# Kernel tuning notes

Measured on AMD Instinct MI355X. Metric: run time of the kernel, lower is better.

The kernel has to match this reference:

```python
import jax, jax.numpy as jnp
import numpy as np

D, H, L, FF, EPS = 3, 3, 12, 2048, 1e-5
B, C, T = 32, 2, 64


def _ln(x, g, b):
    m = jnp.mean(x, -1, keepdims=True)
    v = jnp.mean((x - m) ** 2, -1, keepdims=True)
    return (x - m) / jnp.sqrt(v + EPS) * g + b


def _mha(xq, xkv, w, b, ow, ob):
    # xq: [Tq,B,D], xkv: [S,B,D]; w: [3D,D] packed q/k/v like torch in_proj_weight
    Tq, Bb, _ = xq.shape
    S = xkv.shape[0]
    q = xq @ w[:D].T + b[:D]
    k = xkv @ w[D:2 * D].T + b[D:2 * D]
    v = xkv @ w[2 * D:].T + b[2 * D:]
    dh = D // H  # = 1
    q = q.reshape(Tq, Bb, H, dh)
    k = k.reshape(S, Bb, H, dh)
    v = v.reshape(S, Bb, H, dh)
    scores = jnp.einsum('qbhd,kbhd->bhqk', q, k) * (1.0 / np.sqrt(dh))
    att = jax.nn.softmax(scores, axis=-1)
    o = jnp.einsum('bhqk,kbhd->qbhd', att, v).reshape(Tq, Bb, D)
    return o @ ow.T + ob


def _ffn(x, w1, b1, w2, b2):
    return jax.nn.relu(x @ w1.T + b1) @ w2.T + b2


def _encode(x, p):
    def layer(h, pl):
        aw, ab, aow, aob, g1, b1, g2, b2, f1w, f1b, f2w, f2b = pl
        h = _ln(h + _mha(h, h, aw, ab, aow, aob), g1, b1)
        h = _ln(h + _ffn(h, f1w, f1b, f2w, f2b), g2, b2)
        return h, None
    h, _ = jax.lax.scan(layer, x, p)
    return h


def _decode(tgt, mem, p):
    def layer(h, pl):
        (sw, sb, sow, sob, cw, cb, cow, cob,
         g1, b1, g2, b2, g3, b3, f1w, f1b, f2w, f2b) = pl
        h = _ln(h + _mha(h, h, sw, sb, sow, sob), g1, b1)      # self-attn (no mask, as in source)
        h = _ln(h + _mha(h, mem, cw, cb, cow, cob), g2, b2)    # cross-attn
        h = _ln(h + _ffn(h, f1w, f1b, f2w, f2b), g3, b3)
        return h, None
    h, _ = jax.lax.scan(layer, tgt, p)
    return h


def _forward(src, angle, enc_p, enc_ng, enc_nb, dec_p, dec_ng, dec_nb):
    Bb, _, Tt = src.shape
    a = jnp.broadcast_to(angle.reshape(Bb, 1, 1), (Bb, 1, Tt))
    x = jnp.transpose(jnp.concatenate([src, a], axis=1), (2, 0, 1))  # [T,B,3]
    mem = _ln(_encode(x, enc_p), enc_ng, enc_nb)  # encoder memory is loop-invariant

    def dec(o):
        return _ln(_decode(o, mem, dec_p), dec_ng, dec_nb)

    out = jnp.zeros_like(x).at[0].set(x[0])

    def step(o, t):
        pred = dec(o)
        return o.at[t].set(pred[t]), None

    out, _ = jax.lax.scan(step, out, jnp.arange(1, Tt))
    return jnp.transpose(out, (1, 2, 0))  # [B,3,T]


def setup_inputs() -> dict:
    key = jax.random.key(0)
    it = iter(jax.random.split(key, 40))
    def n(shape, s=0.05):
        return jax.random.normal(next(it), shape, dtype=jnp.float32) * s
    inp = {
        'src': jax.random.normal(next(it), (B, C, T), dtype=jnp.float32),
        'angle': jax.random.normal(next(it), (B,), dtype=jnp.float32),
        'enc_attn_w': n((L, 3 * D, D)), 'enc_attn_b': n((L, 3 * D)),
        'enc_attn_ow': n((L, D, D)), 'enc_attn_ob': n((L, D)),
        'enc_ln1_g': jnp.ones((L, D)), 'enc_ln1_b': jnp.zeros((L, D)),
        'enc_ln2_g': jnp.ones((L, D)), 'enc_ln2_b': jnp.zeros((L, D)),
        'enc_ff1_w': n((L, FF, D)), 'enc_ff1_b': n((L, FF)),
        'enc_ff2_w': n((L, D, FF)), 'enc_ff2_b': n((L, D)),
        'enc_norm_g': jnp.ones((D,)), 'enc_norm_b': jnp.zeros((D,)),
        'dec_sa_w': n((L, 3 * D, D)), 'dec_sa_b': n((L, 3 * D)),
        'dec_sa_ow': n((L, D, D)), 'dec_sa_ob': n((L, D)),
        'dec_ca_w': n((L, 3 * D, D)), 'dec_ca_b': n((L, 3 * D)),
        'dec_ca_ow': n((L, D, D)), 'dec_ca_ob': n((L, D)),
        'dec_ln1_g': jnp.ones((L, D)), 'dec_ln1_b': jnp.zeros((L, D)),
        'dec_ln2_g': jnp.ones((L, D)), 'dec_ln2_b': jnp.zeros((L, D)),
        'dec_ln3_g': jnp.ones((L, D)), 'dec_ln3_b': jnp.zeros((L, D)),
        'dec_ff1_w': n((L, FF, D)), 'dec_ff1_b': n((L, FF)),
        'dec_ff2_w': n((L, D, FF)), 'dec_ff2_b': n((L, D)),
        'dec_norm_g': jnp.ones((D,)), 'dec_norm_b': jnp.zeros((D,)),
    }
    return inp


def reference(src, angle,
              enc_attn_w, enc_attn_b, enc_attn_ow, enc_attn_ob,
              enc_ln1_g, enc_ln1_b, enc_ln2_g, enc_ln2_b,
              enc_ff1_w, enc_ff1_b, enc_ff2_w, enc_ff2_b,
              enc_norm_g, enc_norm_b,
              dec_sa_w, dec_sa_b, dec_sa_ow, dec_sa_ob,
              dec_ca_w, dec_ca_b, dec_ca_ow, dec_ca_ob,
              dec_ln1_g, dec_ln1_b, dec_ln2_g, dec_ln2_b, dec_ln3_g, dec_ln3_b,
              dec_ff1_w, dec_ff1_b, dec_ff2_w, dec_ff2_b,
              dec_norm_g, dec_norm_b):
    enc_p = (enc_attn_w, enc_attn_b, enc_attn_ow, enc_attn_ob,
             enc_ln1_g, enc_ln1_b, enc_ln2_g, enc_ln2_b,
             enc_ff1_w, enc_ff1_b, enc_ff2_w, enc_ff2_b)
    dec_p = (dec_sa_w, dec_sa_b, dec_sa_ow, dec_sa_ob,
             dec_ca_w, dec_ca_b, dec_ca_ow, dec_ca_ob,
             dec_ln1_g, dec_ln1_b, dec_ln2_g, dec_ln2_b, dec_ln3_g, dec_ln3_b,
             dec_ff1_w, dec_ff1_b, dec_ff2_w, dec_ff2_b)
    return _forward(src, angle, enc_p, enc_norm_g, enc_norm_b, dec_p, dec_norm_g, dec_norm_b)
```

## Files before the change

kernel.cpp:

```cpp
#include <hip/hip_runtime.h>

#define DEV static __device__ __forceinline__

typedef _Float16 h2 __attribute__((ext_vector_type(2)));

DEV float fdot2f(h2 a, h2 b, float c) {
#if __has_builtin(__builtin_amdgcn_fdot2)
  return __builtin_amdgcn_fdot2(a, b, c, false);
#else
  return c + (float)a.x * (float)b.x + (float)a.y * (float)b.y;
#endif
}

DEV void ln3(float& a, float& b, float& c, const float* g, const float* bt) {
  float m = (a + b + c) * (1.0f / 3.0f);
  float d0 = a - m, d1 = b - m, d2 = c - m;
  float v = (d0 * d0 + d1 * d1 + d2 * d2) * (1.0f / 3.0f);
  float rs = rsqrtf(v + 1e-5f);
  a = fmaf(d0 * rs, g[0], bt[0]);
  b = fmaf(d1 * rs, g[1], bt[1]);
  c = fmaf(d2 * rs, g[2], bt[2]);
}

DEV unsigned pkh2(float a, float b) {
  h2 v = {(_Float16)a, (_Float16)b};
  return __builtin_bit_cast(unsigned, v);
}

__global__ void __launch_bounds__(256) prepack_kernel(
    const float* ea_w, const float* ea_b, const float* ea_ow, const float* ea_ob,
    const float* el1g, const float* el1b, const float* el2g, const float* el2b,
    const float* ef1w, const float* ef1b, const float* ef2w, const float* ef2b,
    const float* eng, const float* enb,
    const float* dsw, const float* dsb, const float* dsow, const float* dsob,
    const float* dcw, const float* dcb, const float* dcow, const float* dcob,
    const float* dl1g, const float* dl1b, const float* dl2g, const float* dl2b,
    const float* dl3g, const float* dl3b,
    const float* df1w, const float* df1b, const float* df2w, const float* df2b,
    const float* dng, const float* dnb,
    float* ws) {
  const int l = blockIdx.x, tid = threadIdx.x;
  const bool enc = l < 12;
  const int li = enc ? l : l - 12;
  const float* f1w = (enc ? ef1w : df1w) + li * 2048 * 3;
  const float* f1b = (enc ? ef1b : df1b) + li * 2048;
  const float* f2w = (enc ? ef2w : df2w) + li * 3 * 2048;
  uint4* FA4 = (uint4*)ws + (size_t)l * 1024;
  uint4* FB4 = (uint4*)ws + 24 * 1024 + (size_t)l * 1024;
  for (int jp = tid; jp < 1024; jp += 256) {
    const int j0 = jp * 2, j1 = j0 + 1;
    uint4 A;
    A.x = pkh2(f1w[j0 * 3 + 0], f1w[j1 * 3 + 0]);
    A.y = pkh2(f1w[j0 * 3 + 1], f1w[j1 * 3 + 1]);
    A.z = pkh2(f1w[j0 * 3 + 2], f1w[j1 * 3 + 2]);
    A.w = pkh2(f1b[j0], f1b[j1]);
    FA4[jp] = A;
    uint4 Bv;
    Bv.x = pkh2(f2w[j0], f2w[j1]);
    Bv.y = pkh2(f2w[2048 + j0], f2w[2048 + j1]);
    Bv.z = pkh2(f2w[4096 + j0], f2w[4096 + j1]);
    Bv.w = 0u;
    FB4[jp] = Bv;
  }
  float* S = ws + 196608 + l * 128;
  if (tid == 0) {
    const float* aw = (enc ? ea_w : dsw) + li * 27;
    const float* ab = (enc ? ea_b : dsb) + li * 9;
    const float* aow = (enc ? ea_ow : dsow) + li * 9;
    const float* aob = (enc ? ea_ob : dsob) + li * 3;
    for (int i = 0; i < 27; ++i) S[i] = aw[i];
    for (int i = 0; i < 9; ++i) S[27 + i] = ab[i];
    for (int i = 0; i < 9; ++i) S[36 + i] = aow[i];
    for (int i = 0; i < 3; ++i) S[45 + i] = aob[i];
    const float* p;
    p = (enc ? el1g : dl1g) + li * 3; for (int i = 0; i < 3; ++i) S[48 + i] = p[i];
    p = (enc ? el1b : dl1b) + li * 3; for (int i = 0; i < 3; ++i) S[51 + i] = p[i];
    p = (enc ? el2g : dl2g) + li * 3; for (int i = 0; i < 3; ++i) S[54 + i] = p[i];
    p = (enc ? el2b : dl2b) + li * 3; for (int i = 0; i < 3; ++i) S[57 + i] = p[i];
    p = (enc ? ef2b : df2b) + li * 3; for (int i = 0; i < 3; ++i) S[60 + i] = p[i];
    if (!enc) {
      const float* cw = dcw + li * 27;
      for (int i = 0; i < 9; ++i) {
        S[64 + i] = cw[i];
        S[94 + i] = cw[9 + i];
        S[106 + i] = cw[18 + i];
      }
      const float* cb = dcb + li * 9;
      for (int i = 0; i < 3; ++i) {
        S[73 + i] = cb[i];
        S[103 + i] = cb[3 + i];
        S[115 + i] = cb[6 + i];
      }
      for (int i = 0; i < 9; ++i) S[76 + i] = dcow[li * 9 + i];
      for (int i = 0; i < 3; ++i) S[85 + i] = dcob[li * 3 + i];
      p = dl3g + li * 3; for (int i = 0; i < 3; ++i) S[88 + i] = p[i];
      p = dl3b + li * 3; for (int i = 0; i < 3; ++i) S[91 + i] = p[i];
    }
  }
  if (l == 0 && tid == 1) {
    float* G = ws + 196608 + 24 * 128;
    for (int i = 0; i < 3; ++i) {
      G[i] = eng[i]; G[3 + i] = enb[i];
      G[6 + i] = dng[i]; G[9 + i] = dnb[i];
    }
  }
}

template <int NR>
DEV void ffn_core(const uint4* FA, const uint4* FB,
                  const float (&X0)[4], const float (&X1)[4], const float (&X2)[4],
                  float (&acc)[4][3], int lane) {
  h2 xd0[NR], xd1[NR], xd2[NR];
#pragma unroll
  for (int i = 0; i < NR; ++i) {
    xd0[i] = h2{(_Float16)X0[i], (_Float16)X0[i]};
    xd1[i] = h2{(_Float16)X1[i], (_Float16)X1[i]};
    xd2[i] = h2{(_Float16)X2[i], (_Float16)X2[i]};
  }
#pragma unroll
  for (int i = 0; i < NR; ++i) { acc[i][0] = 0.f; acc[i][1] = 0.f; acc[i][2] = 0.f; }
  const h2 z = {(_Float16)0, (_Float16)0};
#pragma unroll 4
  for (int kk = 0; kk < 16; ++kk) {
    const int jp = lane + (kk << 6);
    uint4 a = FA[jp];
    uint4 c = FB[jp];
    h2 wa0 = __builtin_bit_cast(h2, a.x), wa1 = __builtin_bit_cast(h2, a.y);
    h2 wa2 = __builtin_bit_cast(h2, a.z), bb = __builtin_bit_cast(h2, a.w);
    h2 wc0 = __builtin_bit_cast(h2, c.x), wc1 = __builtin_bit_cast(h2, c.y);
    h2 wc2 = __builtin_bit_cast(h2, c.z);
#pragma unroll
    for (int i = 0; i < NR; ++i) {
      h2 t = wa0 * xd0[i] + wa1 * xd1[i] + wa2 * xd2[i] + bb;
      t = __builtin_elementwise_max(t, z);
      acc[i][0] = fdot2f(wc0, t, acc[i][0]);
      acc[i][1] = fdot2f(wc1, t, acc[i][1]);
      acc[i][2] = fdot2f(wc2, t, acc[i][2]);
    }
  }
#pragma unroll
  for (int m = 1; m < 64; m <<= 1) {
#pragma unroll
    for (int i = 0; i < NR; ++i) {
      acc[i][0] += __shfl_xor(acc[i][0], m, 64);
      acc[i][1] += __shfl_xor(acc[i][1], m, 64);
      acc[i][2] += __shfl_xor(acc[i][2], m, 64);
    }
  }
}

template <bool DEC>
DEV void run_layer(const float* sm, const uint4* FA, const uint4* FB,
                   const float (*ckv)[8],
                   float (*h)[5], float (*hln)[5], float* kvq,
                   float (*p1)[25], float (*p2)[25],
                   float (*o_s)[5], const float* glob,
                   int R, int t, bool from_os, bool wpred,
                   int wave, int lane, int tid) {
  {
    const int r = tid >> 4, o = tid & 15;
    if (r < R && o <= 9) {
      float x0, x1, x2;
      if (DEC && from_os) {
        const bool real = r < t;
        x0 = real ? o_s[r][0] : 0.f;
        x1 = real ? o_s[r][1] : 0.f;
        x2 = real ? o_s[r][2] : 0.f;
      } else {
        x0 = h[r][0]; x1 = h[r][1]; x2 = h[r][2];
      }
      if (o < 9) {
        float v = fmaf(sm[o * 3], x0,
                  fmaf(sm[o * 3 + 1], x1, fmaf(sm[o * 3 + 2], x2, sm[27 + o])));
        kvq[r * 13 + o + o / 3] = v;
      } else {
        kvq[r * 13 + 7] = (DEC && r == R - 1 && t > 0) ? (float)(64 - t) : 1.0f;
        if (DEC && from_os) { h[r][0] = x0; h[r][1] = x1; h[r][2] = x2; }
      }
    }
    if (DEC && o == 9 && r >= R) kvq[r * 13 + 7] = 0.f;
  }
  __syncthreads();
  if (wave < 12) {
    const int hd = wave % 3, c = wave / 3;
    const int p0 = c * 16;
    float den = 0.f, num = 0.f;
    if (p0 < R) {
      const float q = kvq[lane * 13 + hd] * 1.44269504f;
#pragma unroll
      for (int pp = 0; pp < 16; ++pp) {
        const int p = p0 + pp;
        float e = exp2f(q * kvq[p * 13 + 4 + hd]);
        if (DEC) e *= kvq[p * 13 + 7];
        den += e;
        num = fmaf(e, kvq[p * 13 + 8 + hd], num);
      }
    }
    p1[lane][2 * wave] = den;
    p1[lane][2 * wave + 1] = num;
  }
  __syncthreads();
  if (DEC) {
    if (wave < 12) {
      const int r = lane, hd = wave % 3, c = wave / 3;
      float d0 = p1[r][0] + p1[r][6] + p1[r][12] + p1[r][18];
      float n0 = p1[r][1] + p1[r][7] + p1[r][13] + p1[r][19];
      float d1 = p1[r][2] + p1[r][8] + p1[r][14] + p1[r][20];
      float n1 = p1[r][3] + p1[r][9] + p1[r][15] + p1[r][21];
      float d2 = p1[r][4] + p1[r][10] + p1[r][16] + p1[r][22];
      float n2 = p1[r][5] + p1[r][11] + p1[r][17] + p1[r][23];
      float oh0 = __fdividef(n0, d0), oh1 = __fdividef(n1, d1), oh2 = __fdividef(n2, d2);
      float a0 = fmaf(sm[36], oh0, fmaf(sm[37], oh1, fmaf(sm[38], oh2, sm[45]))) + h[r][0];
      float a1 = fmaf(sm[39], oh0, fmaf(sm[40], oh1, fmaf(sm[41], oh2, sm[46]))) + h[r][1];
      float a2 = fmaf(sm[42], oh0, fmaf(sm[43], oh1, fmaf(sm[44], oh2, sm[47]))) + h[r][2];
      ln3(a0, a1, a2, sm + 48, sm + 51);
      if (wave == 0 && r < R) { hln[r][0] = a0; hln[r][1] = a1; hln[r][2] = a2; }
      float q = fmaf(sm[64 + hd * 3], a0,
                fmaf(sm[64 + hd * 3 + 1], a1,
                fmaf(sm[64 + hd * 3 + 2], a2, sm[73 + hd]))) * 1.44269504f;
      const int p0 = c * 16;
      float den = 0.f, num = 0.f;
#pragma unroll
      for (int pp = 0; pp < 16; ++pp) {
        const int p = p0 + pp;
        float e = exp2f(q * ckv[p][hd]);
        den += e;
        num = fmaf(e, ckv[p][3 + hd], num);
      }
      p2[r][2 * wave] = den;
      p2[r][2 * wave + 1] = num;
    }
    __syncthreads();
  }
  {
    const int nr = (wave < R) ? (1 + (R - 1 - wave) / 16) : 0;
    if (nr > 0) {
      const float(*pp)[25] = DEC ? p2 : p1;
      const float* ow = DEC ? sm + 76 : sm + 36;
      const float* ob = DEC ? sm + 85 : sm + 45;
      const float* lg = DEC ? sm + 54 : sm + 48;
      const float* lb = DEC ? sm + 57 : sm + 51;
      float X0[4], X1[4], X2[4];
#pragma unroll
      for (int i = 0; i < 4; ++i) {
        X0[i] = 0.f; X1[i] = 0.f; X2[i] = 0.f;
        if (i < nr) {
          const int rc = wave + 16 * i;
          float d0 = pp[rc][0] + pp[rc][6] + pp[rc][12] + pp[rc][18];
          float n0 = pp[rc][1] + pp[rc][7] + pp[rc][13] + pp[rc][19];
          float d1 = pp[rc][2] + pp[rc][8] + pp[rc][14] + pp[rc][20];
          float n1 = pp[rc][3] + pp[rc][9] + pp[rc][15] + pp[rc][21];
          float d2 = pp[rc][4] + pp[rc][10] + pp[rc][16] + pp[rc][22];
          float n2 = pp[rc][5] + pp[rc][11] + pp[rc][17] + pp[rc][23];
          float oh0 = __fdividef(n0, d0), oh1 = __fdividef(n1, d1), oh2 = __fdividef(n2, d2);
          float hr0, hr1, hr2;
          if (DEC) { hr0 = hln[rc][0]; hr1 = hln[rc][1]; hr2 = hln[rc][2]; }
          else     { hr0 = h[rc][0];   hr1 = h[rc][1];   hr2 = h[rc][2]; }
          float a0 = fmaf(ow[0], oh0, fmaf(ow[1], oh1, fmaf(ow[2], oh2, ob[0]))) + hr0;
          float a1 = fmaf(ow[3], oh0, fmaf(ow[4], oh1, fmaf(ow[5], oh2, ob[1]))) + hr1;
          float a2 = fmaf(ow[6], oh0, fmaf(ow[7], oh1, fmaf(ow[8], oh2, ob[2]))) + hr2;
          ln3(a0, a1, a2, lg, lb);
          X0[i] = a0; X1[i] = a1; X2[i] = a2;
        }
      }
      float acc[4][3];
      switch (nr) {
        case 1: ffn_core<1>(FA, FB, X0, X1, X2, acc, lane); break;
        case 2: ffn_core<2>(FA, FB, X0, X1, X2, acc, lane); break;
        case 3: ffn_core<3>(FA, FB, X0, X1, X2, acc, lane); break;
        default: ffn_core<4>(FA, FB, X0, X1, X2, acc, lane); break;
      }
      if (lane == 0) {
        const float* fg = DEC ? sm + 88 : sm + 54;
        const float* fb = DEC ? sm + 91 : sm + 57;
#pragma unroll
        for (int i = 0; i < 4; ++i) {
          if (i < nr) {
            const int r = wave + 16 * i;
            float y0 = acc[i][0] + sm[60] + X0[i];
            float y1 = acc[i][1] + sm[61] + X1[i];
            float y2 = acc[i][2] + sm[62] + X2[i];
            ln3(y0, y1, y2, fg, fb);
            h[r][0] = y0; h[r][1] = y1; h[r][2] = y2;
            if (DEC && wpred && r == R - 1) {
              ln3(y0, y1, y2, glob + 6, glob + 9);
              o_s[t][0] = y0; o_s[t][1] = y1; o_s[t][2] = y2;
            }
          }
        }
      }
    }
    __syncthreads();
  }
}

__global__ void __launch_bounds__(1024) tf_kernel(const float* src, const float* angle,
                                                  const float* ws, float* out) {
  __shared__ float small_s[24][128];
  __shared__ float glob[16];
  __shared__ float h[64][5];
  __shared__ float hln[64][5];
  __shared__ float kvq[64 * 13];
  __shared__ float part1[64][25];
  __shared__ float part2[64][25];
  __shared__ float o_s[64][5];
  __shared__ float ckcv[12][64][8];
  const int b = blockIdx.x;
  const int tid = threadIdx.x, wave = tid >> 6, lane = tid & 63;
  const uint4* FA = (const uint4*)ws;
  const uint4* FB = (const uint4*)ws + 24 * 1024;
  const float* SM = ws + 196608;
  const float* GB = SM + 24 * 128;
  for (int i = tid; i < 24 * 128; i += 1024) ((float*)small_s)[i] = SM[i];
  if (tid < 16) glob[tid] = GB[tid];
  if (tid < 64) {
    float x0 = src[b * 128 + tid];
    float x1 = src[b * 128 + 64 + tid];
    float x2 = angle[b];
    h[tid][0] = x0; h[tid][1] = x1; h[tid][2] = x2;
    o_s[tid][0] = (tid == 0) ? x0 : 0.f;
    o_s[tid][1] = (tid == 0) ? x1 : 0.f;
    o_s[tid][2] = (tid == 0) ? x2 : 0.f;
  }
  __syncthreads();
  for (int l = 0; l < 12; ++l)
    run_layer<false>(small_s[l], FA + (size_t)l * 1024, FB + (size_t)l * 1024,
                     nullptr, h, hln, kvq, part1, part2, o_s, glob,
                     64, 0, false, false, wave, lane, tid);
  if (tid < 64) {
    float a = h[tid][0], bb = h[tid][1], c = h[tid][2];
    ln3(a, bb, c, glob + 0, glob + 3);
    h[tid][0] = a; h[tid][1] = bb; h[tid][2] = c;
  }
  __syncthreads();
  if (wave < 12) {
    const float* sm = small_s[12 + wave];
    float m0 = h[lane][0], m1 = h[lane][1], m2 = h[lane][2];
    float k0 = fmaf(sm[94], m0, fmaf(sm[95], m1, fmaf(sm[96], m2, sm[103])));
    float k1 = fmaf(sm[97], m0, fmaf(sm[98], m1, fmaf(sm[99], m2, sm[104])));
    float k2 = fmaf(sm[100], m0, fmaf(sm[101], m1, fmaf(sm[102], m2, sm[105])));
    float v0 = fmaf(sm[106], m0, fmaf(sm[107], m1, fmaf(sm[108], m2, sm[115])));
    float v1 = fmaf(sm[109], m0, fmaf(sm[110], m1, fmaf(sm[111], m2, sm[116])));
    float v2 = fmaf(sm[112], m0, fmaf(sm[113], m1, fmaf(sm[114], m2, sm[117])));
    ckcv[wave][lane][0] = k0; ckcv[wave][lane][1] = k1; ckcv[wave][lane][2] = k2;
    ckcv[wave][lane][3] = v0; ckcv[wave][lane][4] = v1; ckcv[wave][lane][5] = v2;
  }
  __syncthreads();
  for (int t = 1; t < 64; ++t) {
    const int R = t + 1;
    for (int l = 0; l < 12; ++l)
      run_layer<true>(small_s[12 + l], FA + (size_t)(12 + l) * 1024,
                      FB + (size_t)(12 + l) * 1024, ckcv[l],
                      h, hln, kvq, part1, part2, o_s, glob, R, t,
                      l == 0, l == 11, wave, lane, tid);
  }
  if (tid < 192) {
    int d = tid / 64, tt = tid % 64;
    out[b * 192 + tid] = o_s[tt][d];
  }
}

extern "C" void kernel_launch(void* const* d_in, const int* in_sizes, int n_in,
                              void* d_out, int out_size, void* d_ws, size_t ws_size,
                              hipStream_t stream) {
  (void)in_sizes; (void)n_in; (void)out_size; (void)ws_size;
  float* ws = (float*)d_ws;
  prepack_kernel<<<24, 256, 0, stream>>>(
      (const float*)d_in[2], (const float*)d_in[3], (const float*)d_in[4], (const float*)d_in[5],
      (const float*)d_in[6], (const float*)d_in[7], (const float*)d_in[8], (const float*)d_in[9],
      (const float*)d_in[10], (const float*)d_in[11], (const float*)d_in[12], (const float*)d_in[13],
      (const float*)d_in[14], (const float*)d_in[15],
      (const float*)d_in[16], (const float*)d_in[17], (const float*)d_in[18], (const float*)d_in[19],
      (const float*)d_in[20], (const float*)d_in[21], (const float*)d_in[22], (const float*)d_in[23],
      (const float*)d_in[24], (const float*)d_in[25], (const float*)d_in[26], (const float*)d_in[27],
      (const float*)d_in[28], (const float*)d_in[29],
      (const float*)d_in[30], (const float*)d_in[31], (const float*)d_in[32], (const float*)d_in[33],
      (const float*)d_in[34], (const float*)d_in[35],
      ws);
  tf_kernel<<<32, 1024, 0, stream>>>((const float*)d_in[0], (const float*)d_in[1], ws,
                                     (float*)d_out);
}
```

Baseline: 6.353 ms.

## Double-buffer FFN weights in LDS with async global-to-LDS prefetch of next layer

Interleaves each layer's packed FFN weight arrays (FA/FB) into one contiguous 2048-entry block in the workspace. Each layer now starts an asynchronous global_load_lds copy of the next layer's block into the other half of a two-slot shared-memory buffer. The FFN core then reads weights from LDS instead of global/L2. This hides weight fetch latency behind the attention and FFN work of the current layer. In exchange it adds 64KB of LDS per block, and correctness depends on the existing barriers waiting for the async LDS writes to finish.

```diff
diff --git a/kernel.cpp b/kernel.cpp
--- a/kernel.cpp
+++ b/kernel.cpp
@@ -45,8 +45,8 @@
   const float* f1w = (enc ? ef1w : df1w) + li * 2048 * 3;
   const float* f1b = (enc ? ef1b : df1b) + li * 2048;
   const float* f2w = (enc ? ef2w : df2w) + li * 3 * 2048;
-  uint4* FA4 = (uint4*)ws + (size_t)l * 1024;
-  uint4* FB4 = (uint4*)ws + 24 * 1024 + (size_t)l * 1024;
+  uint4* FA4 = (uint4*)ws + (size_t)l * 2048;
+  uint4* FB4 = FA4 + 1024;
   for (int jp = tid; jp < 1024; jp += 256) {
     const int j0 = jp * 2, j1 = j0 + 1;
     uint4 A;
@@ -106,8 +106,24 @@
   }
 }
 
+DEV void stage_fab(const uint4* g, uint4* l, int wave, int lane) {
+#if __has_builtin(__builtin_amdgcn_global_load_lds)
+  const int e0 = wave * 64;
+  __builtin_amdgcn_global_load_lds(
+      (const __attribute__((address_space(1))) void*)(g + e0 + lane),
+      (__attribute__((address_space(3))) void*)(l + e0), 16, 0, 0);
+  const int e1 = 1024 + wave * 64;
+  __builtin_amdgcn_global_load_lds(
+      (const __attribute__((address_space(1))) void*)(g + e1 + lane),
+      (__attribute__((address_space(3))) void*)(l + e1), 16, 0, 0);
+#else
+  l[wave * 64 + lane] = g[wave * 64 + lane];
+  l[1024 + wave * 64 + lane] = g[1024 + wave * 64 + lane];
+#endif
+}
+
 template <int NR>
-DEV void ffn_core(const uint4* FA, const uint4* FB,
+DEV void ffn_core(const uint4* FAB,
                   const float (&X0)[4], const float (&X1)[4], const float (&X2)[4],
                   float (&acc)[4][3], int lane) {
   h2 xd0[NR], xd1[NR], xd2[NR];
@@ -123,8 +139,8 @@
 #pragma unroll 4
   for (int kk = 0; kk < 16; ++kk) {
     const int jp = lane + (kk << 6);
-    uint4 a = FA[jp];
-    uint4 c = FB[jp];
+    uint4 a = FAB[jp];
+    uint4 c = FAB[1024 + jp];
     h2 wa0 = __builtin_bit_cast(h2, a.x), wa1 = __builtin_bit_cast(h2, a.y);
     h2 wa2 = __builtin_bit_cast(h2, a.z), bb = __builtin_bit_cast(h2, a.w);
     h2 wc0 = __builtin_bit_cast(h2, c.x), wc1 = __builtin_bit_cast(h2, c.y);
@@ -150,13 +166,15 @@
 }
 
 template <bool DEC>
-DEV void run_layer(const float* sm, const uint4* FA, const uint4* FB,
+DEV void run_layer(const float* sm, const uint4* FAB,
+                   const uint4* stage_src, uint4* stage_dst,
                    const float (*ckv)[8],
                    float (*h)[5], float (*hln)[5], float* kvq,
                    float (*p1)[25], float (*p2)[25],
                    float (*o_s)[5], const float* glob,
                    int R, int t, bool from_os, bool wpred,
                    int wave, int lane, int tid) {
+  stage_fab(stage_src, stage_dst, wave, lane);
   {
     const int r = tid >> 4, o = tid & 15;
     if (r < R && o <= 9) {
@@ -265,10 +283,10 @@
       }
       float acc[4][3];
       switch (nr) {
-        case 1: ffn_core<1>(FA, FB, X0, X1, X2, acc, lane); break;
-        case 2: ffn_core<2>(FA, FB, X0, X1, X2, acc, lane); break;
-        case 3: ffn_core<3>(FA, FB, X0, X1, X2, acc, lane); break;
-        default: ffn_core<4>(FA, FB, X0, X1, X2, acc, lane); break;
+        case 1: ffn_core<1>(FAB, X0, X1, X2, acc, lane); break;
+        case 2: ffn_core<2>(FAB, X0, X1, X2, acc, lane); break;
+        case 3: ffn_core<3>(FAB, X0, X1, X2, acc, lane); break;
+        default: ffn_core<4>(FAB, X0, X1, X2, acc, lane); break;
       }
       if (lane == 0) {
         const float* fg = DEC ? sm + 88 : sm + 54;
@@ -296,6 +314,7 @@
 
 __global__ void __launch_bounds__(1024) tf_kernel(const float* src, const float* angle,
                                                   const float* ws, float* out) {
+  __shared__ uint4 fbuf[2][2048];
   __shared__ float small_s[24][128];
   __shared__ float glob[16];
   __shared__ float h[64][5];
@@ -307,10 +326,10 @@
   __shared__ float ckcv[12][64][8];
   const int b = blockIdx.x;
   const int tid = threadIdx.x, wave = tid >> 6, lane = tid & 63;
-  const uint4* FA = (const uint4*)ws;
-  const uint4* FB = (const uint4*)ws + 24 * 1024;
+  const uint4* FABg = (const uint4*)ws;
   const float* SM = ws + 196608;
   const float* GB = SM + 24 * 128;
+  stage_fab(FABg, fbuf[0], wave, lane);
   for (int i = tid; i < 24 * 128; i += 1024) ((float*)small_s)[i] = SM[i];
   if (tid < 16) glob[tid] = GB[tid];
   if (tid < 64) {
@@ -323,10 +342,15 @@
     o_s[tid][2] = (tid == 0) ? x2 : 0.f;
   }
   __syncthreads();
-  for (int l = 0; l < 12; ++l)
-    run_layer<false>(small_s[l], FA + (size_t)l * 1024, FB + (size_t)l * 1024,
-                     nullptr, h, hln, kvq, part1, part2, o_s, glob,
+  int cc = 0;
+  for (int l = 0; l < 12; ++l) {
+    const int nxt = (l < 11) ? l + 1 : 12;
+    run_layer<false>(small_s[l], fbuf[cc & 1], FABg + (size_t)nxt * 2048,
+                     fbuf[(cc + 1) & 1], nullptr,
+                     h, hln, kvq, part1, part2, o_s, glob,
                      64, 0, false, false, wave, lane, tid);
+    ++cc;
+  }
   if (tid < 64) {
     float a = h[tid][0], bb = h[tid][1], c = h[tid][2];
     ln3(a, bb, c, glob + 0, glob + 3);
@@ -348,11 +372,14 @@
   __syncthreads();
   for (int t = 1; t < 64; ++t) {
     const int R = t + 1;
-    for (int l = 0; l < 12; ++l)
-      run_layer<true>(small_s[12 + l], FA + (size_t)(12 + l) * 1024,
-                      FB + (size_t)(12 + l) * 1024, ckcv[l],
+    for (int li = 0; li < 12; ++li) {
+      const int nxt = (li < 11) ? 12 + li + 1 : 12;
+      run_layer<true>(small_s[12 + li], fbuf[cc & 1], FABg + (size_t)nxt * 2048,
+                      fbuf[(cc + 1) & 1], ckcv[li],
                       h, hln, kvq, part1, part2, o_s, glob, R, t,
-                      l == 0, l == 11, wave, lane, tid);
+                      li == 0, li == 11, wave, lane, tid);
+      ++cc;
+    }
   }
   if (tid < 192) {
     int d = tid / 64, tt = tid % 64;
```

New measurement: 6.463 ms. Within noise of the previous version (+1.7%).

## Restructure attention to 4 waves, batch FFN over 8 waves with more rows

Applied to the files above, without the earlier changes.

Attention now uses 4 waves that each handle all three heads over a 16-key slice, reading keys and values as float4 from transposed shared buffers. The output projection and LayerNorm are computed once by a single wave into a shared buffer, instead of being recomputed per FFN wave. The FFN then runs on 8 waves, each holding up to 8 rows, so every weight load is reused across more rows, and the FA/FB weights are interleaved per layer for locality. The cost is fewer active waves for the FFN weight streaming, plus an extra barrier and serialized single-wave work per layer.

```diff
diff --git a/kernel.cpp b/kernel.cpp
--- a/kernel.cpp
+++ b/kernel.cpp
@@ -45,8 +45,8 @@
   const float* f1w = (enc ? ef1w : df1w) + li * 2048 * 3;
   const float* f1b = (enc ? ef1b : df1b) + li * 2048;
   const float* f2w = (enc ? ef2w : df2w) + li * 3 * 2048;
-  uint4* FA4 = (uint4*)ws + (size_t)l * 1024;
-  uint4* FB4 = (uint4*)ws + 24 * 1024 + (size_t)l * 1024;
+  uint4* FA4 = (uint4*)ws + (size_t)l * 2048;
+  uint4* FB4 = FA4 + 1024;
   for (int jp = tid; jp < 1024; jp += 256) {
     const int j0 = jp * 2, j1 = j0 + 1;
     uint4 A;
@@ -107,9 +107,9 @@
 }
 
 template <int NR>
-DEV void ffn_core(const uint4* FA, const uint4* FB,
-                  const float (&X0)[4], const float (&X1)[4], const float (&X2)[4],
-                  float (&acc)[4][3], int lane) {
+DEV void ffn_core(const uint4* FA,
+                  const float (&X0)[8], const float (&X1)[8], const float (&X2)[8],
+                  float (&acc)[8][3], int lane) {
   h2 xd0[NR], xd1[NR], xd2[NR];
 #pragma unroll
   for (int i = 0; i < NR; ++i) {
@@ -124,7 +124,7 @@
   for (int kk = 0; kk < 16; ++kk) {
     const int jp = lane + (kk << 6);
     uint4 a = FA[jp];
-    uint4 c = FB[jp];
+    uint4 c = FA[1024 + jp];
     h2 wa0 = __builtin_bit_cast(h2, a.x), wa1 = __builtin_bit_cast(h2, a.y);
     h2 wa2 = __builtin_bit_cast(h2, a.z), bb = __builtin_bit_cast(h2, a.w);
     h2 wc0 = __builtin_bit_cast(h2, c.x), wc1 = __builtin_bit_cast(h2, c.y);
@@ -150,133 +150,158 @@
 }
 
 template <bool DEC>
-DEV void run_layer(const float* sm, const uint4* FA, const uint4* FB,
-                   const float (*ckv)[8],
-                   float (*h)[5], float (*hln)[5], float* kvq,
-                   float (*p1)[25], float (*p2)[25],
+DEV void run_layer(const float* sm, const uint4* FA, const float4* ckv4,
+                   float (*h)[5], float (*hln)[5], float (*xs)[5],
+                   float (*kq)[5], float4* kvk, float4* kvv,
+                   float (*p1t)[64], float (*p2t)[64],
                    float (*o_s)[5], const float* glob,
                    int R, int t, bool from_os, bool wpred,
                    int wave, int lane, int tid) {
   {
     const int r = tid >> 4, o = tid & 15;
-    if (r < R && o <= 9) {
-      float x0, x1, x2;
-      if (DEC && from_os) {
-        const bool real = r < t;
-        x0 = real ? o_s[r][0] : 0.f;
-        x1 = real ? o_s[r][1] : 0.f;
-        x2 = real ? o_s[r][2] : 0.f;
-      } else {
-        x0 = h[r][0]; x1 = h[r][1]; x2 = h[r][2];
-      }
-      if (o < 9) {
+    if (o < 9) {
+      if (r < R) {
+        float x0, x1, x2;
+        if (DEC && from_os) {
+          const bool real = r < t;
+          x0 = real ? o_s[r][0] : 0.f;
+          x1 = real ? o_s[r][1] : 0.f;
+          x2 = real ? o_s[r][2] : 0.f;
+        } else {
+          x0 = h[r][0]; x1 = h[r][1]; x2 = h[r][2];
+        }
         float v = fmaf(sm[o * 3], x0,
                   fmaf(sm[o * 3 + 1], x1, fmaf(sm[o * 3 + 2], x2, sm[27 + o])));
-        kvq[r * 13 + o + o / 3] = v;
-      } else {
-        kvq[r * 13 + 7] = (DEC && r == R - 1 && t > 0) ? (float)(64 - t) : 1.0f;
-        if (DEC && from_os) { h[r][0] = x0; h[r][1] = x1; h[r][2] = x2; }
-      }
-    }
-    if (DEC && o == 9 && r >= R) kvq[r * 13 + 7] = 0.f;
-  }
-  __syncthreads();
-  if (wave < 12) {
-    const int hd = wave % 3, c = wave / 3;
-    const int p0 = c * 16;
-    float den = 0.f, num = 0.f;
-    if (p0 < R) {
-      const float q = kvq[lane * 13 + hd] * 1.44269504f;
+        if (o < 3) kq[r][o] = v;
+        else if (o < 6) ((float*)&kvk[r])[o - 3] = v;
+        else ((float*)&kvv[r])[o - 6] = v;
+      } else if (DEC) {
+        if (o < 3) kq[r][o] = 0.f;
+        else if (o < 6) ((float*)&kvk[r])[o - 3] = 0.f;
+        else ((float*)&kvv[r])[o - 6] = 0.f;
+      }
+    } else if (o == 9) {
+      if (DEC)
+        ((float*)&kvk[r])[3] =
+            (r == R - 1 && t > 0) ? (float)(64 - t) : (r < R ? 1.f : 0.f);
+      if (DEC && from_os && r < R) {
+        const bool real = r < t;
+        h[r][0] = real ? o_s[r][0] : 0.f;
+        h[r][1] = real ? o_s[r][1] : 0.f;
+        h[r][2] = real ? o_s[r][2] : 0.f;
+      }
+    }
+  }
+  __syncthreads();
+  if (wave < 4) {
+    const float l2e = 1.44269504f;
+    float q0 = kq[lane][0] * l2e, q1 = kq[lane][1] * l2e, q2 = kq[lane][2] * l2e;
+    float d0 = 0.f, n0 = 0.f, d1 = 0.f, n1 = 0.f, d2 = 0.f, n2 = 0.f;
+    const int p0 = wave * 16;
+#pragma unroll
+    for (int pp = 0; pp < 16; ++pp) {
+      float4 k = kvk[p0 + pp], v = kvv[p0 + pp];
+      float e0 = exp2f(q0 * k.x), e1 = exp2f(q1 * k.y), e2 = exp2f(q2 * k.z);
+      if (DEC) { e0 *= k.w; e1 *= k.w; e2 *= k.w; }
+      d0 += e0; n0 = fmaf(e0, v.x, n0);
+      d1 += e1; n1 = fmaf(e1, v.y, n1);
+      d2 += e2; n2 = fmaf(e2, v.z, n2);
+    }
+    p1t[wave * 6 + 0][lane] = d0; p1t[wave * 6 + 1][lane] = n0;
+    p1t[wave * 6 + 2][lane] = d1; p1t[wave * 6 + 3][lane] = n1;
+    p1t[wave * 6 + 4][lane] = d2; p1t[wave * 6 + 5][lane] = n2;
+  }
+  __syncthreads();
+  if (DEC) {
+    if (wave < 4) {
+      float d0 = p1t[0][lane] + p1t[6][lane] + p1t[12][lane] + p1t[18][lane];
+      float n0 = p1t[1][lane] + p1t[7][lane] + p1t[13][lane] + p1t[19][lane];
+      float d1 = p1t[2][lane] + p1t[8][lane] + p1t[14][lane] + p1t[20][lane];
+      float n1 = p1t[3][lane] + p1t[9][lane] + p1t[15][lane] + p1t[21][lane];
+      float d2 = p1t[4][lane] + p1t[10][lane] + p1t[16][lane] + p1t[22][lane];
+      float n2 = p1t[5][lane] + p1t[11][lane] + p1t[17][lane] + p1t[23][lane];
+      float oh0 = __fdividef(n0, d0), oh1 = __fdividef(n1, d1), oh2 = __fdividef(n2, d2);
+      float a0 = fmaf(sm[36], oh0, fmaf(sm[37], oh1, fmaf(sm[38], oh2, sm[45]))) + h[lane][0];
+      float a1 = fmaf(sm[39], oh0, fmaf(sm[40], oh1, fmaf(sm[41], oh2, sm[46]))) + h[lane][1];
+      float a2 = fmaf(sm[42], oh0, fmaf(sm[43], oh1, fmaf(sm[44], oh2, sm[47]))) + h[lane][2];
+      ln3(a0, a1, a2, sm + 48, sm + 51);
+      if (wave == 0 && lane < R) {
+        hln[lane][0] = a0; hln[lane][1] = a1; hln[lane][2] = a2;
+      }
+      const float l2e = 1.44269504f;
+      float q0 = fmaf(sm[64], a0, fmaf(sm[65], a1, fmaf(sm[66], a2, sm[73]))) * l2e;
+      float q1 = fmaf(sm[67], a0, fmaf(sm[68], a1, fmaf(sm[69], a2, sm[74]))) * l2e;
+      float q2 = fmaf(sm[70], a0, fmaf(sm[71], a1, fmaf(sm[72], a2, sm[75]))) * l2e;
+      float D0 = 0.f, N0 = 0.f, D1 = 0.f, N1 = 0.f, D2 = 0.f, N2 = 0.f;
+      const int p0 = wave * 16;
 #pragma unroll
       for (int pp = 0; pp < 16; ++pp) {
-        const int p = p0 + pp;
-        float e = exp2f(q * kvq[p * 13 + 4 + hd]);
-        if (DEC) e *= kvq[p * 13 + 7];
-        den += e;
-        num = fmaf(e, kvq[p * 13 + 8 + hd], num);
-      }
-    }
-    p1[lane][2 * wave] = den;
-    p1[lane][2 * wave + 1] = num;
-  }
-  __syncthreads();
-  if (DEC) {
-    if (wave < 12) {
-      const int r = lane, hd = wave % 3, c = wave / 3;
-      float d0 = p1[r][0] + p1[r][6] + p1[r][12] + p1[r][18];
-      float n0 = p1[r][1] + p1[r][7] + p1[r][13] + p1[r][19];
-      float d1 = p1[r][2] + p1[r][8] + p1[r][14] + p1[r][20];
-      float n1 = p1[r][3] + p1[r][9] + p1[r][15] + p1[r][21];
-      float d2 = p1[r][4] + p1[r][10] + p1[r][16] + p1[r][22];
-      float n2 = p1[r][5] + p1[r][11] + p1[r][17] + p1[r][23];
-      float oh0 = __fdividef(n0, d0), oh1 = __fdividef(n1, d1), oh2 = __fdividef(n2, d2);
-      float a0 = fmaf(sm[36], oh0, fmaf(sm[37], oh1, fmaf(sm[38], oh2, sm[45]))) + h[r][0];
-      float a1 = fmaf(sm[39], oh0, fmaf(sm[40], oh1, fmaf(sm[41], oh2, sm[46]))) + h[r][1];
-      float a2 = fmaf(sm[42], oh0, fmaf(sm[43], oh1, fmaf(sm[44], oh2, sm[47]))) + h[r][2];
-      ln3(a0, a1, a2, sm + 48, sm + 51);
-      if (wave == 0 && r < R) { hln[r][0] = a0; hln[r][1] = a1; hln[r][2] = a2; }
-      float q = fmaf(sm[64 + hd * 3], a0,
-                fmaf(sm[64 + hd * 3 + 1], a1,
-                fmaf(sm[64 + hd * 3 + 2], a2, sm[73 + hd]))) * 1.44269504f;
-      const int p0 = c * 16;
-      float den = 0.f, num = 0.f;
-#pragma unroll
-      for (int pp = 0; pp < 16; ++pp) {
-        const int p = p0 + pp;
-        float e = exp2f(q * ckv[p][hd]);
-        den += e;
-        num = fmaf(e, ckv[p][3 + hd], num);
-      }
-      p2[r][2 * wave] = den;
-      p2[r][2 * wave + 1] = num;
+        float4 k = ckv4[(p0 + pp) * 2], v = ckv4[(p0 + pp) * 2 + 1];
+        float e0 = exp2f(q0 * k.x), e1 = exp2f(q1 * k.y), e2 = exp2f(q2 * k.z);
+        D0 += e0; N0 = fmaf(e0, v.x, N0);
+        D1 += e1; N1 = fmaf(e1, v.y, N1);
+        D2 += e2; N2 = fmaf(e2, v.z, N2);
+      }
+      p2t[wave * 6 + 0][lane] = D0; p2t[wave * 6 + 1][lane] = N0;
+      p2t[wave * 6 + 2][lane] = D1; p2t[wave * 6 + 3][lane] = N1;
+      p2t[wave * 6 + 4][lane] = D2; p2t[wave * 6 + 5][lane] = N2;
     }
     __syncthreads();
   }
+  if (wave == 0) {
+    const float (*pt)[64] = DEC ? p2t : p1t;
+    float d0 = pt[0][lane] + pt[6][lane] + pt[12][lane] + pt[18][lane];
+    float n0 = pt[1][lane] + pt[7][lane] + pt[13][lane] + pt[19][lane];
+    float d1 = pt[2][lane] + pt[8][lane] + pt[14][lane] + pt[20][lane];
+    float n1 = pt[3][lane] + pt[9][lane] + pt[15][lane] + pt[21][lane];
+    float d2 = pt[4][lane] + pt[10][lane] + pt[16][lane] + pt[22][lane];
+    float n2 = pt[5][lane] + pt[11][lane] + pt[17][lane] + pt[23][lane];
+    float oh0 = __fdividef(n0, d0), oh1 = __fdividef(n1, d1), oh2 = __fdividef(n2, d2);
+    const float* ow = DEC ? sm + 76 : sm + 36;
+    const float* ob = DEC ? sm + 85 : sm + 45;
+    float r0, r1, r2;
+    if (DEC) { r0 = hln[lane][0]; r1 = hln[lane][1]; r2 = hln[lane][2]; }
+    else     { r0 = h[lane][0];   r1 = h[lane][1];   r2 = h[lane][2]; }
+    float a0 = fmaf(ow[0], oh0, fmaf(ow[1], oh1, fmaf(ow[2], oh2, ob[0]))) + r0;
+    float a1 = fmaf(ow[3], oh0, fmaf(ow[4], oh1, fmaf(ow[5], oh2, ob[1]))) + r1;
+    float a2 = fmaf(ow[6], oh0, fmaf(ow[7], oh1, fmaf(ow[8], oh2, ob[2]))) + r2;
+    const float* lg = DEC ? sm + 54 : sm + 48;
+    const float* lb = DEC ? sm + 57 : sm + 51;
+    ln3(a0, a1, a2, lg, lb);
+    if (lane < R) { xs[lane][0] = a0; xs[lane][1] = a1; xs[lane][2] = a2; }
+  }
+  __syncthreads();
   {
-    const int nr = (wave < R) ? (1 + (R - 1 - wave) / 16) : 0;
-    if (nr > 0) {
-      const float(*pp)[25] = DEC ? p2 : p1;
-      const float* ow = DEC ? sm + 76 : sm + 36;
-      const float* ob = DEC ? sm + 85 : sm + 45;
-      const float* lg = DEC ? sm + 54 : sm + 48;
-      const float* lb = DEC ? sm + 57 : sm + 51;
-      float X0[4], X1[4], X2[4];
-#pragma unroll
-      for (int i = 0; i < 4; ++i) {
-        X0[i] = 0.f; X1[i] = 0.f; X2[i] = 0.f;
+    if (wave < 8 && wave < R) {
+      const int nr = (R - wave + 7) >> 3;
+      float X0[8], X1[8], X2[8];
+#pragma unroll
+      for (int i = 0; i < 8; ++i) {
         if (i < nr) {
-          const int rc = wave + 16 * i;
-          float d0 = pp[rc][0] + pp[rc][6] + pp[rc][12] + pp[rc][18];
-          float n0 = pp[rc][1] + pp[rc][7] + pp[rc][13] + pp[rc][19];
-          float d1 = pp[rc][2] + pp[rc][8] + pp[rc][14] + pp[rc][20];
-          float n1 = pp[rc][3] + pp[rc][9] + pp[rc][15] + pp[rc][21];
-          float d2 = pp[rc][4] + pp[rc][10] + pp[rc][16] + pp[rc][22];
-          float n2 = pp[rc][5] + pp[rc][11] + pp[rc][17] + pp[rc][23];
-          float oh0 = __fdividef(n0, d0), oh1 = __fdividef(n1, d1), oh2 = __fdividef(n2, d2);
-          float hr0, hr1, hr2;
-          if (DEC) { hr0 = hln[rc][0]; hr1 = hln[rc][1]; hr2 = hln[rc][2]; }
-          else     { hr0 = h[rc][0];   hr1 = h[rc][1];   hr2 = h[rc][2]; }
-          float a0 = fmaf(ow[0], oh0, fmaf(ow[1], oh1, fmaf(ow[2], oh2, ob[0]))) + hr0;
-          float a1 = fmaf(ow[3], oh0, fmaf(ow[4], oh1, fmaf(ow[5], oh2, ob[1]))) + hr1;
-          float a2 = fmaf(ow[6], oh0, fmaf(ow[7], oh1, fmaf(ow[8], oh2, ob[2]))) + hr2;
-          ln3(a0, a1, a2, lg, lb);
-          X0[i] = a0; X1[i] = a1; X2[i] = a2;
+          const int rc = wave + 8 * i;
+          X0[i] = xs[rc][0]; X1[i] = xs[rc][1]; X2[i] = xs[rc][2];
+        } else {
+          X0[i] = 0.f; X1[i] = 0.f; X2[i] = 0.f;
         }
       }
-      float acc[4][3];
+      float acc[8][3];
       switch (nr) {
-        case 1: ffn_core<1>(FA, FB, X0, X1, X2, acc, lane); break;
-        case 2: ffn_core<2>(FA, FB, X0, X1, X2, acc, lane); break;
-        case 3: ffn_core<3>(FA, FB, X0, X1, X2, acc, lane); break;
-        default: ffn_core<4>(FA, FB, X0, X1, X2, acc, lane); break;
+        case 1: ffn_core<1>(FA, X0, X1, X2, acc, lane); break;
+        case 2: ffn_core<2>(FA, X0, X1, X2, acc, lane); break;
+        case 3: ffn_core<3>(FA, X0, X1, X2, acc, lane); break;
+        case 4: ffn_core<4>(FA, X0, X1, X2, acc, lane); break;
+        case 5: ffn_core<5>(FA, X0, X1, X2, acc, lane); break;
+        case 6: ffn_core<6>(FA, X0, X1, X2, acc, lane); break;
+        case 7: ffn_core<7>(FA, X0, X1, X2, acc, lane); break;
+        default: ffn_core<8>(FA, X0, X1, X2, acc, lane); break;
       }
       if (lane == 0) {
         const float* fg = DEC ? sm + 88 : sm + 54;
         const float* fb = DEC ? sm + 91 : sm + 57;
 #pragma unroll
-        for (int i = 0; i < 4; ++i) {
+        for (int i = 0; i < 8; ++i) {
           if (i < nr) {
-            const int r = wave + 16 * i;
+            const int r = wave + 8 * i;
             float y0 = acc[i][0] + sm[60] + X0[i];
             float y1 = acc[i][1] + sm[61] + X1[i];
             float y2 = acc[i][2] + sm[62] + X2[i];
@@ -300,15 +325,17 @@
   __shared__ float glob[16];
   __shared__ float h[64][5];
   __shared__ float hln[64][5];
-  __shared__ float kvq[64 * 13];
-  __shared__ float part1[64][25];
-  __shared__ float part2[64][25];
+  __shared__ float xs[64][5];
   __shared__ float o_s[64][5];
-  __shared__ float ckcv[12][64][8];
+  __shared__ float kq[64][5];
+  __shared__ __align__(16) float4 kvk[64];
+  __shared__ __align__(16) float4 kvv[64];
+  __shared__ float p1t[24][64];
+  __shared__ float p2t[24][64];
+  __shared__ __align__(16) float ckcv[12][64][8];
   const int b = blockIdx.x;
   const int tid = threadIdx.x, wave = tid >> 6, lane = tid & 63;
-  const uint4* FA = (const uint4*)ws;
-  const uint4* FB = (const uint4*)ws + 24 * 1024;
+  const uint4* FABg = (const uint4*)ws;
   const float* SM = ws + 196608;
   const float* GB = SM + 24 * 128;
   for (int i = tid; i < 24 * 128; i += 1024) ((float*)small_s)[i] = SM[i];
@@ -324,8 +351,8 @@
   }
   __syncthreads();
   for (int l = 0; l < 12; ++l)
-    run_layer<false>(small_s[l], FA + (size_t)l * 1024, FB + (size_t)l * 1024,
-                     nullptr, h, hln, kvq, part1, part2, o_s, glob,
+    run_layer<false>(small_s[l], FABg + (size_t)l * 2048, nullptr,
+                     h, hln, xs, kq, kvk, kvv, p1t, p2t, o_s, glob,
                      64, 0, false, false, wave, lane, tid);
   if (tid < 64) {
     float a = h[tid][0], bb = h[tid][1], c = h[tid][2];
@@ -343,16 +370,18 @@
     float v1 = fmaf(sm[109], m0, fmaf(sm[110], m1, fmaf(sm[111], m2, sm[116])));
     float v2 = fmaf(sm[112], m0, fmaf(sm[113], m1, fmaf(sm[114], m2, sm[117])));
     ckcv[wave][lane][0] = k0; ckcv[wave][lane][1] = k1; ckcv[wave][lane][2] = k2;
-    ckcv[wave][lane][3] = v0; ckcv[wave][lane][4] = v1; ckcv[wave][lane][5] = v2;
+    ckcv[wave][lane][3] = 0.f;
+    ckcv[wave][lane][4] = v0; ckcv[wave][lane][5] = v1; ckcv[wave][lane][6] = v2;
+    ckcv[wave][lane][7] = 0.f;
   }
   __syncthreads();
   for (int t = 1; t < 64; ++t) {
     const int R = t + 1;
-    for (int l = 0; l < 12; ++l)
-      run_layer<true>(small_s[12 + l], FA + (size_t)(12 + l) * 1024,
-                      FB + (size_t)(12 + l) * 1024, ckcv[l],
-                      h, hln, kvq, part1, part2, o_s, glob, R, t,
-                      l == 0, l == 11, wave, lane, tid);
+    for (int li = 0; li < 12; ++li)
+      run_layer<true>(small_s[12 + li], FABg + (size_t)(12 + li) * 2048,
+                      (const float4*)ckcv[li],
+                      h, hln, xs, kq, kvk, kvv, p1t, p2t, o_s, glob, R, t,
+                      li == 0, li == 11, wave, lane, tid);
   }
   if (tid < 192) {
     int d = tid / 64, tt = tid % 64;
```

Measured after the change: 7.575 ms. 19.2% more time.

## Fuse QKV projection into attention waves and drop a barrier per layer

Applied to the files above, without the earlier changes.

Removes the separate QKV projection phase and its __syncthreads by having each attention wave recompute its query, key and value from the hidden state on the fly. Stores the hidden state as float4 for vectorized shared loads. Interleaves the two FFN weight tables per layer into one contiguous region for locality. This trades redundant per-lane projection arithmetic for one fewer barrier per layer across 12×64 layer passes, and the first decoder layer now also has wave 12 write the masked hidden state.

```diff
diff --git a/kernel.cpp b/kernel.cpp
--- a/kernel.cpp
+++ b/kernel.cpp
@@ -45,8 +45,8 @@
   const float* f1w = (enc ? ef1w : df1w) + li * 2048 * 3;
   const float* f1b = (enc ? ef1b : df1b) + li * 2048;
   const float* f2w = (enc ? ef2w : df2w) + li * 3 * 2048;
-  uint4* FA4 = (uint4*)ws + (size_t)l * 1024;
-  uint4* FB4 = (uint4*)ws + 24 * 1024 + (size_t)l * 1024;
+  uint4* FA4 = (uint4*)ws + (size_t)l * 2048;
+  uint4* FB4 = FA4 + 1024;
   for (int jp = tid; jp < 1024; jp += 256) {
     const int j0 = jp * 2, j1 = j0 + 1;
     uint4 A;
@@ -107,7 +107,7 @@
 }
 
 template <int NR>
-DEV void ffn_core(const uint4* FA, const uint4* FB,
+DEV void ffn_core(const uint4* FA,
                   const float (&X0)[4], const float (&X1)[4], const float (&X2)[4],
                   float (&acc)[4][3], int lane) {
   h2 xd0[NR], xd1[NR], xd2[NR];
@@ -124,7 +124,7 @@
   for (int kk = 0; kk < 16; ++kk) {
     const int jp = lane + (kk << 6);
     uint4 a = FA[jp];
-    uint4 c = FB[jp];
+    uint4 c = FA[1024 + jp];
     h2 wa0 = __builtin_bit_cast(h2, a.x), wa1 = __builtin_bit_cast(h2, a.y);
     h2 wa2 = __builtin_bit_cast(h2, a.z), bb = __builtin_bit_cast(h2, a.w);
     h2 wc0 = __builtin_bit_cast(h2, c.x), wc1 = __builtin_bit_cast(h2, c.y);
@@ -150,54 +150,72 @@
 }
 
 template <bool DEC>
-DEV void run_layer(const float* sm, const uint4* FA, const uint4* FB,
-                   const float (*ckv)[8],
-                   float (*h)[5], float (*hln)[5], float* kvq,
+DEV void run_layer(const float* sm, const uint4* FA, const float (*ckv)[8],
+                   float4* hv, float (*hln)[5],
                    float (*p1)[25], float (*p2)[25],
                    float (*o_s)[5], const float* glob,
                    int R, int t, bool from_os, bool wpred,
                    int wave, int lane, int tid) {
-  {
-    const int r = tid >> 4, o = tid & 15;
-    if (r < R && o <= 9) {
-      float x0, x1, x2;
-      if (DEC && from_os) {
-        const bool real = r < t;
-        x0 = real ? o_s[r][0] : 0.f;
-        x1 = real ? o_s[r][1] : 0.f;
-        x2 = real ? o_s[r][2] : 0.f;
-      } else {
-        x0 = h[r][0]; x1 = h[r][1]; x2 = h[r][2];
-      }
-      if (o < 9) {
-        float v = fmaf(sm[o * 3], x0,
-                  fmaf(sm[o * 3 + 1], x1, fmaf(sm[o * 3 + 2], x2, sm[27 + o])));
-        kvq[r * 13 + o + o / 3] = v;
-      } else {
-        kvq[r * 13 + 7] = (DEC && r == R - 1 && t > 0) ? (float)(64 - t) : 1.0f;
-        if (DEC && from_os) { h[r][0] = x0; h[r][1] = x1; h[r][2] = x2; }
-      }
-    }
-    if (DEC && o == 9 && r >= R) kvq[r * 13 + 7] = 0.f;
-  }
-  __syncthreads();
   if (wave < 12) {
     const int hd = wave % 3, c = wave / 3;
     const int p0 = c * 16;
+    const float l2e = 1.44269504f;
+    float xq0, xq1, xq2;
+    if (DEC && from_os) {
+      const bool real = lane < t;
+      xq0 = real ? o_s[lane][0] : 0.f;
+      xq1 = real ? o_s[lane][1] : 0.f;
+      xq2 = real ? o_s[lane][2] : 0.f;
+    } else {
+      float4 hx = hv[lane];
+      xq0 = hx.x; xq1 = hx.y; xq2 = hx.z;
+    }
+    float q = fmaf(sm[hd * 3], xq0,
+              fmaf(sm[hd * 3 + 1], xq1,
+              fmaf(sm[hd * 3 + 2], xq2, sm[27 + hd]))) * l2e;
     float den = 0.f, num = 0.f;
-    if (p0 < R) {
-      const float q = kvq[lane * 13 + hd] * 1.44269504f;
-#pragma unroll
-      for (int pp = 0; pp < 16; ++pp) {
-        const int p = p0 + pp;
-        float e = exp2f(q * kvq[p * 13 + 4 + hd]);
-        if (DEC) e *= kvq[p * 13 + 7];
-        den += e;
-        num = fmaf(e, kvq[p * 13 + 8 + hd], num);
-      }
+#pragma unroll
+    for (int pp = 0; pp < 16; ++pp) {
+      const int p = p0 + pp;
+      float x0, x1, x2, mult;
+      if (DEC && from_os) {
+        const bool real = p < t;
+        x0 = real ? o_s[p][0] : 0.f;
+        x1 = real ? o_s[p][1] : 0.f;
+        x2 = real ? o_s[p][2] : 0.f;
+        mult = (p == R - 1) ? (float)(64 - t) : (p < R ? 1.f : 0.f);
+      } else if (DEC) {
+        const int pc = min(p, R - 1);
+        float4 hx = hv[pc];
+        x0 = hx.x; x1 = hx.y; x2 = hx.z;
+        mult = (p == R - 1) ? (t > 0 ? (float)(64 - t) : 1.f)
+                            : (p < R ? 1.f : 0.f);
+      } else {
+        float4 hx = hv[p];
+        x0 = hx.x; x1 = hx.y; x2 = hx.z;
+        mult = 1.f;
+      }
+      float k = fmaf(sm[9 + hd * 3], x0,
+                fmaf(sm[9 + hd * 3 + 1], x1,
+                fmaf(sm[9 + hd * 3 + 2], x2, sm[30 + hd])));
+      float v = fmaf(sm[18 + hd * 3], x0,
+                fmaf(sm[18 + hd * 3 + 1], x1,
+                fmaf(sm[18 + hd * 3 + 2], x2, sm[33 + hd])));
+      float e = exp2f(q * k);
+      if (DEC) e *= mult;
+      den += e;
+      num = fmaf(e, v, num);
     }
     p1[lane][2 * wave] = den;
     p1[lane][2 * wave + 1] = num;
+  } else if (DEC && from_os && wave == 12) {
+    const bool real = lane < t;
+    float4 hx;
+    hx.x = real ? o_s[lane][0] : 0.f;
+    hx.y = real ? o_s[lane][1] : 0.f;
+    hx.z = real ? o_s[lane][2] : 0.f;
+    hx.w = 0.f;
+    hv[lane] = hx;
   }
   __syncthreads();
   if (DEC) {
@@ -210,9 +228,10 @@
       float d2 = p1[r][4] + p1[r][10] + p1[r][16] + p1[r][22];
       float n2 = p1[r][5] + p1[r][11] + p1[r][17] + p1[r][23];
       float oh0 = __fdividef(n0, d0), oh1 = __fdividef(n1, d1), oh2 = __fdividef(n2, d2);
-      float a0 = fmaf(sm[36], oh0, fmaf(sm[37], oh1, fmaf(sm[38], oh2, sm[45]))) + h[r][0];
-      float a1 = fmaf(sm[39], oh0, fmaf(sm[40], oh1, fmaf(sm[41], oh2, sm[46]))) + h[r][1];
-      float a2 = fmaf(sm[42], oh0, fmaf(sm[43], oh1, fmaf(sm[44], oh2, sm[47]))) + h[r][2];
+      float4 hx = hv[r];
+      float a0 = fmaf(sm[36], oh0, fmaf(sm[37], oh1, fmaf(sm[38], oh2, sm[45]))) + hx.x;
+      float a1 = fmaf(sm[39], oh0, fmaf(sm[40], oh1, fmaf(sm[41], oh2, sm[46]))) + hx.y;
+      float a2 = fmaf(sm[42], oh0, fmaf(sm[43], oh1, fmaf(sm[44], oh2, sm[47]))) + hx.z;
       ln3(a0, a1, a2, sm + 48, sm + 51);
       if (wave == 0 && r < R) { hln[r][0] = a0; hln[r][1] = a1; hln[r][2] = a2; }
       float q = fmaf(sm[64 + hd * 3], a0,
@@ -255,7 +274,7 @@
           float oh0 = __fdividef(n0, d0), oh1 = __fdividef(n1, d1), oh2 = __fdividef(n2, d2);
           float hr0, hr1, hr2;
           if (DEC) { hr0 = hln[rc][0]; hr1 = hln[rc][1]; hr2 = hln[rc][2]; }
-          else     { hr0 = h[rc][0];   hr1 = h[rc][1];   hr2 = h[rc][2]; }
+          else     { float4 hx = hv[rc]; hr0 = hx.x; hr1 = hx.y; hr2 = hx.z; }
           float a0 = fmaf(ow[0], oh0, fmaf(ow[1], oh1, fmaf(ow[2], oh2, ob[0]))) + hr0;
           float a1 = fmaf(ow[3], oh0, fmaf(ow[4], oh1, fmaf(ow[5], oh2, ob[1]))) + hr1;
           float a2 = fmaf(ow[6], oh0, fmaf(ow[7], oh1, fmaf(ow[8], oh2, ob[2]))) + hr2;
@@ -265,10 +284,10 @@
       }
       float acc[4][3];
       switch (nr) {
-        case 1: ffn_core<1>(FA, FB, X0, X1, X2, acc, lane); break;
-        case 2: ffn_core<2>(FA, FB, X0, X1, X2, acc, lane); break;
-        case 3: ffn_core<3>(FA, FB, X0, X1, X2, acc, lane); break;
-        default: ffn_core<4>(FA, FB, X0, X1, X2, acc, lane); break;
+        case 1: ffn_core<1>(FA, X0, X1, X2, acc, lane); break;
+        case 2: ffn_core<2>(FA, X0, X1, X2, acc, lane); break;
+        case 3: ffn_core<3>(FA, X0, X1, X2, acc, lane); break;
+        default: ffn_core<4>(FA, X0, X1, X2, acc, lane); break;
       }
       if (lane == 0) {
         const float* fg = DEC ? sm + 88 : sm + 54;
@@ -281,7 +300,8 @@
             float y1 = acc[i][1] + sm[61] + X1[i];
             float y2 = acc[i][2] + sm[62] + X2[i];
             ln3(y0, y1, y2, fg, fb);
-            h[r][0] = y0; h[r][1] = y1; h[r][2] = y2;
+            float4 hx; hx.x = y0; hx.y = y1; hx.z = y2; hx.w = 0.f;
+            hv[r] = hx;
             if (DEC && wpred && r == R - 1) {
               ln3(y0, y1, y2, glob + 6, glob + 9);
               o_s[t][0] = y0; o_s[t][1] = y1; o_s[t][2] = y2;
@@ -298,17 +318,15 @@
                                                   const float* ws, float* out) {
   __shared__ float small_s[24][128];
   __shared__ float glob[16];
-  __shared__ float h[64][5];
+  __shared__ __align__(16) float4 hv[64];
   __shared__ float hln[64][5];
-  __shared__ float kvq[64 * 13];
-  __shared__ float part1[64][25];
-  __shared__ float part2[64][25];
+  __shared__ float p1[64][25];
+  __shared__ float p2[64][25];
   __shared__ float o_s[64][5];
   __shared__ float ckcv[12][64][8];
   const int b = blockIdx.x;
   const int tid = threadIdx.x, wave = tid >> 6, lane = tid & 63;
-  const uint4* FA = (const uint4*)ws;
-  const uint4* FB = (const uint4*)ws + 24 * 1024;
+  const uint4* FABg = (const uint4*)ws;
   const float* SM = ws + 196608;
   const float* GB = SM + 24 * 128;
   for (int i = tid; i < 24 * 128; i += 1024) ((float*)small_s)[i] = SM[i];
@@ -317,25 +335,29 @@
     float x0 = src[b * 128 + tid];
     float x1 = src[b * 128 + 64 + tid];
     float x2 = angle[b];
-    h[tid][0] = x0; h[tid][1] = x1; h[tid][2] = x2;
+    float4 hx; hx.x = x0; hx.y = x1; hx.z = x2; hx.w = 0.f;
+    hv[tid] = hx;
     o_s[tid][0] = (tid == 0) ? x0 : 0.f;
     o_s[tid][1] = (tid == 0) ? x1 : 0.f;
     o_s[tid][2] = (tid == 0) ? x2 : 0.f;
   }
   __syncthreads();
   for (int l = 0; l < 12; ++l)
-    run_layer<false>(small_s[l], FA + (size_t)l * 1024, FB + (size_t)l * 1024,
-                     nullptr, h, hln, kvq, part1, part2, o_s, glob,
+    run_layer<false>(small_s[l], FABg + (size_t)l * 2048, nullptr,
+                     hv, hln, p1, p2, o_s, glob,
                      64, 0, false, false, wave, lane, tid);
   if (tid < 64) {
-    float a = h[tid][0], bb = h[tid][1], c = h[tid][2];
+    float4 hx = hv[tid];
+    float a = hx.x, bb = hx.y, c = hx.z;
     ln3(a, bb, c, glob + 0, glob + 3);
-    h[tid][0] = a; h[tid][1] = bb; h[tid][2] = c;
+    hx.x = a; hx.y = bb; hx.z = c;
+    hv[tid] = hx;
   }
   __syncthreads();
   if (wave < 12) {
     const float* sm = small_s[12 + wave];
-    float m0 = h[lane][0], m1 = h[lane][1], m2 = h[lane][2];
+    float4 hx = hv[lane];
+    float m0 = hx.x, m1 = hx.y, m2 = hx.z;
     float k0 = fmaf(sm[94], m0, fmaf(sm[95], m1, fmaf(sm[96], m2, sm[103])));
     float k1 = fmaf(sm[97], m0, fmaf(sm[98], m1, fmaf(sm[99], m2, sm[104])));
     float k2 = fmaf(sm[100], m0, fmaf(sm[101], m1, fmaf(sm[102], m2, sm[105])));
@@ -348,11 +370,11 @@
   __syncthreads();
   for (int t = 1; t < 64; ++t) {
     const int R = t + 1;
-    for (int l = 0; l < 12; ++l)
-      run_layer<true>(small_s[12 + l], FA + (size_t)(12 + l) * 1024,
-                      FB + (size_t)(12 + l) * 1024, ckcv[l],
-                      h, hln, kvq, part1, part2, o_s, glob, R, t,
-                      l == 0, l == 11, wave, lane, tid);
+    for (int li = 0; li < 12; ++li)
+      run_layer<true>(small_s[12 + li], FABg + (size_t)(12 + li) * 2048,
+                      (const float(*)[8])ckcv[li],
+                      hv, hln, p1, p2, o_s, glob, R, t,
+                      li == 0, li == 11, wave, lane, tid);
   }
   if (tid < 192) {
     int d = tid / 64, tt = tid % 64;
```

Measured after the change: 7.634 ms. 20.2% more time.
